# Performance work log

Hardware: AMD Instinct MI355X
Metric: run time of the kernel (lower is better)

Reference implementation:

```python
import jax, jax.numpy as jnp
from jax import lax
import numpy as np

B, T, C, H = 1024, 512, 32, 256


def _gru_cell(x, h, Wih, Whh, bih, bhh):
    # PyTorch GRU gate math. x: (B, C_in), h: (B, H)
    gi = x @ Wih.T + bih          # (B, 3H)
    gh = h @ Whh.T + bhh          # (B, 3H)
    i_r, i_z, i_n = jnp.split(gi, 3, axis=-1)
    h_r, h_z, h_n = jnp.split(gh, 3, axis=-1)
    r = jax.nn.sigmoid(i_r + h_r)
    z = jax.nn.sigmoid(i_z + h_z)
    n = jnp.tanh(i_n + r * h_n)
    return (1.0 - z) * n + z * h


def setup_inputs() -> dict:
    key = jax.random.key(0)
    ks = jax.random.split(key, 12)
    s = 0.08  # ~ uniform(-1/sqrt(H)) scale
    return {
        "x": jax.random.normal(ks[0], (B, T, C), dtype=jnp.float32),
        "enc_Wih": jax.random.normal(ks[1], (3 * H, C), dtype=jnp.float32) * s,
        "enc_Whh": jax.random.normal(ks[2], (3 * H, H), dtype=jnp.float32) * s,
        "enc_bih": jax.random.normal(ks[3], (3 * H,), dtype=jnp.float32) * s,
        "enc_bhh": jax.random.normal(ks[4], (3 * H,), dtype=jnp.float32) * s,
        "dec_Wih": jax.random.normal(ks[5], (3 * H, C), dtype=jnp.float32) * s,
        "dec_Whh": jax.random.normal(ks[6], (3 * H, H), dtype=jnp.float32) * s,
        "dec_bih": jax.random.normal(ks[7], (3 * H,), dtype=jnp.float32) * s,
        "dec_bhh": jax.random.normal(ks[8], (3 * H,), dtype=jnp.float32) * s,
        "proj_W": jax.random.normal(ks[9], (C, H), dtype=jnp.float32) * s,
        "proj_b": jax.random.normal(ks[10], (C,), dtype=jnp.float32) * s,
    }


def reference(x, enc_Wih, enc_Whh, enc_bih, enc_bhh,
              dec_Wih, dec_Whh, dec_bih, dec_bhh, proj_W, proj_b):
    batch = x.shape[0]
    h0 = jnp.zeros((batch, H), dtype=x.dtype)

    # ---- encoder: scan over time, keep only final hidden ----
    xs = jnp.swapaxes(x, 0, 1)  # (T, B, C)

    def enc_step(h, xt):
        return _gru_cell(xt, h, enc_Wih, enc_Whh, enc_bih, enc_bhh), None

    h_enc, _ = lax.scan(enc_step, h0, xs)

    start = jnp.zeros((batch, C), dtype=x.dtype)

    def dec_step(carry, _):
        h, prev = carry
        h_new = _gru_cell(prev, h, dec_Wih, dec_Whh, dec_bih, dec_bhh)
        pred = h_new @ proj_W.T + proj_b  # (B, C)
        return (h_new, pred), pred

    _, preds = lax.scan(dec_step, (h_enc, start), None, length=T)
    return jnp.swapaxes(preds, 0, 1)  # (B, T, C)
```

## Files before the change

kernel.cpp:

```cpp
#include <hip/hip_runtime.h>

typedef short bf16x8 __attribute__((ext_vector_type(8)));
typedef float f32x4 __attribute__((ext_vector_type(4)));

#define MFMA16(a, b, c) __builtin_amdgcn_mfma_f32_16x16x32_bf16(a, b, c, 0, 0, 0)

#define T_ 512
#define C_ 32
#define H_ 256

__device__ __forceinline__ unsigned short f2bf(float f) {
  union { float f; unsigned u; } v; v.f = f;
  return (unsigned short)((v.u + 0x7fffu + ((v.u >> 16) & 1u)) >> 16);
}
__device__ __forceinline__ float fsigmoid(float x) {
  float e = __builtin_amdgcn_exp2f(-1.442695041f * x);
  return __builtin_amdgcn_rcpf(1.0f + e);
}
__device__ __forceinline__ float ftanh(float x) {
  float e = __builtin_amdgcn_exp2f(2.885390082f * x);
  return 1.0f - 2.0f * __builtin_amdgcn_rcpf(e + 1.0f);
}

__global__ void pack_kernel(
    const float* __restrict__ encWih, const float* __restrict__ encWhh,
    const float* __restrict__ encbih, const float* __restrict__ encbhh,
    const float* __restrict__ decWih, const float* __restrict__ decWhh,
    const float* __restrict__ decbih, const float* __restrict__ decbhh,
    const float* __restrict__ projW, const float* __restrict__ projB,
    unsigned short* __restrict__ encW, unsigned short* __restrict__ decW,
    unsigned short* __restrict__ pW, float* __restrict__ encBias,
    float* __restrict__ decBias, float* __restrict__ pB) {
  int i = blockIdx.x * 256 + threadIdx.x;
  if (i < 768 * 288) {
    int n = i / 288, k = i % 288;
    float ve = (k < 32) ? encWih[n * 32 + k] : encWhh[n * 256 + k - 32];
    float vd = (k < 32) ? decWih[n * 32 + k] : decWhh[n * 256 + k - 32];
    encW[i] = f2bf(ve);
    decW[i] = f2bf(vd);
  }
  if (i < 32 * 256) pW[i] = f2bf(projW[i]);
  if (i < 256) {
    encBias[i]       = encbih[i] + encbhh[i];
    encBias[256 + i] = encbih[256 + i] + encbhh[256 + i];
    encBias[512 + i] = encbih[512 + i];
    encBias[768 + i] = encbhh[512 + i];
    decBias[i]       = decbih[i] + decbhh[i];
    decBias[256 + i] = decbih[256 + i] + decbhh[256 + i];
    decBias[512 + i] = decbih[512 + i];
    decBias[768 + i] = decbhh[512 + i];
  }
  if (i < 32) pB[i] = projB[i];
}

__global__ __launch_bounds__(1024) void gru_kernel(
    const float* __restrict__ x,
    const unsigned short* __restrict__ encW,
    const unsigned short* __restrict__ decW,
    const unsigned short* __restrict__ pW,
    const float* __restrict__ encBias,
    const float* __restrict__ decBias,
    const float* __restrict__ pB,
    float* __restrict__ out) {
  __shared__ __align__(16) unsigned short wnl[6][256][40];
  __shared__ __align__(16) unsigned short h_lds[2][16][264];
  __shared__ __align__(16) unsigned short xb[2][16][40];
  __shared__ __align__(16) unsigned short pwl[32][264];

  const int tid = (int)threadIdx.x;
  const int wave = tid >> 6, lane = tid & 63;
  const int l15 = lane & 15, l4 = lane >> 4;
  const int ko = l4 * 8;
  const int gbase = (int)blockIdx.x * 16;
  const int j = wave * 16 + l15;

  for (int i = tid; i < 2 * 16 * 264 / 2; i += 1024) ((unsigned*)h_lds)[i] = 0;
  for (int i = tid; i < 2 * 16 * 40 / 2; i += 1024) ((unsigned*)xb)[i] = 0;
  {
    int n = tid >> 5, slot = tid & 31;
    *(bf16x8*)&pwl[n][slot * 8] = *(const bf16x8*)(pW + n * 256 + slot * 8);
  }

  const float* xLane = x + (size_t)(gbase + (tid >> 5)) * (T_ * C_) + (tid & 31);
  float* outLane = out + (size_t)(gbase + l4 * 4) * (T_ * C_) + wave * 16 + l15;
  const float pbias = (wave < 2) ? pB[wave * 16 + l15] : 0.f;
  f32x4 hreg = {0.f, 0.f, 0.f, 0.f};

  bf16x8 wi0, wi1, wi2, wr[8], wz[8], wn2[2];

  auto loadW = [&](const unsigned short* Wp) {
    wi0 = *(const bf16x8*)(Wp + (size_t)j * 288 + ko);
    wi1 = *(const bf16x8*)(Wp + (size_t)(j + 256) * 288 + ko);
    wi2 = *(const bf16x8*)(Wp + (size_t)(j + 512) * 288 + ko);
#pragma unroll
    for (int kk = 0; kk < 8; ++kk) {
      wr[kk] = *(const bf16x8*)(Wp + (size_t)j * 288 + 32 + kk * 32 + ko);
      wz[kk] = *(const bf16x8*)(Wp + (size_t)(j + 256) * 288 + 32 + kk * 32 + ko);
    }
#pragma unroll
    for (int kk = 0; kk < 2; ++kk)
      wn2[kk] = *(const bf16x8*)(Wp + (size_t)(j + 512) * 288 + 32 + kk * 32 + ko);
    for (int i = tid; i < 6 * 256 * 4; i += 1024) {
      int kc = i >> 10, rem = i & 1023;
      int jj = rem >> 2, kc2 = rem & 3;
      *(bf16x8*)&wnl[kc][jj][kc2 * 8] =
          *(const bf16x8*)(Wp + (size_t)(jj + 512) * 288 + 32 + (kc + 2) * 32 + kc2 * 8);
    }
  };

  loadW(encW);
  float br = encBias[j], bz = encBias[256 + j];
  float bin = encBias[512 + j], bhn = encBias[768 + j];
  if (tid < 512) xb[0][tid >> 5][tid & 31] = f2bf(xLane[0]);
  __syncthreads();

  for (int t = 0; t < T_; ++t) {
    if (t < T_ - 1 && tid < 512)
      xb[(t + 1) & 1][tid >> 5][tid & 31] = f2bf(xLane[(size_t)(t + 1) * C_]);

    f32x4 accr = {br, br, br, br}, accz = {bz, bz, bz, bz};
    f32x4 accin = {bin, bin, bin, bin}, acchn = {bhn, bhn, bhn, bhn};
    {
      bf16x8 a0 = *(const bf16x8*)&xb[t & 1][l15][ko];
      accr  = MFMA16(a0, wi0, accr);
      accz  = MFMA16(a0, wi1, accz);
      accin = MFMA16(a0, wi2, accin);
    }
#pragma unroll
    for (int kk = 0; kk < 8; ++kk) {
      bf16x8 ah = *(const bf16x8*)&h_lds[t & 1][l15][kk * 32 + ko];
      accr = MFMA16(ah, wr[kk], accr);
      accz = MFMA16(ah, wz[kk], accz);
      bf16x8 wnk = (kk < 2) ? wn2[kk] : *(const bf16x8*)&wnl[kk - 2][j][ko];
      acchn = MFMA16(ah, wnk, acchn);
    }
#pragma unroll
    for (int r = 0; r < 4; ++r) {
      float rg = fsigmoid(accr[r]);
      float zg = fsigmoid(accz[r]);
      float ng = ftanh(accin[r] + rg * acchn[r]);
      float hv = zg * (hreg[r] - ng) + ng;
      hreg[r] = hv;
      h_lds[(t + 1) & 1][l4 * 4 + r][j] = f2bf(hv);
    }
    __syncthreads();
  }

  loadW(decW);
  br = decBias[j]; bz = decBias[256 + j];
  bin = decBias[512 + j]; bhn = decBias[768 + j];
  if (tid < 320) ((unsigned*)xb)[tid] = 0;
  __syncthreads();

  for (int t = 0; t < T_; ++t) {
    f32x4 accr = {br, br, br, br}, accz = {bz, bz, bz, bz};
    f32x4 accin = {bin, bin, bin, bin}, acchn = {bhn, bhn, bhn, bhn};
    {
      bf16x8 a0 = *(const bf16x8*)&xb[0][l15][ko];
      accr  = MFMA16(a0, wi0, accr);
      accz  = MFMA16(a0, wi1, accz);
      accin = MFMA16(a0, wi2, accin);
    }
#pragma unroll
    for (int kk = 0; kk < 8; ++kk) {
      bf16x8 ah = *(const bf16x8*)&h_lds[t & 1][l15][kk * 32 + ko];
      accr = MFMA16(ah, wr[kk], accr);
      accz = MFMA16(ah, wz[kk], accz);
      bf16x8 wnk = (kk < 2) ? wn2[kk] : *(const bf16x8*)&wnl[kk - 2][j][ko];
      acchn = MFMA16(ah, wnk, acchn);
    }
#pragma unroll
    for (int r = 0; r < 4; ++r) {
      float rg = fsigmoid(accr[r]);
      float zg = fsigmoid(accz[r]);
      float ng = ftanh(accin[r] + rg * acchn[r]);
      float hv = zg * (hreg[r] - ng) + ng;
      hreg[r] = hv;
      h_lds[(t + 1) & 1][l4 * 4 + r][j] = f2bf(hv);
    }
    __syncthreads();

    if (wave < 2) {
      f32x4 pa = {pbias, pbias, pbias, pbias};
#pragma unroll
      for (int kk = 0; kk < 8; ++kk) {
        bf16x8 ah = *(const bf16x8*)&h_lds[(t + 1) & 1][l15][kk * 32 + ko];
        bf16x8 bw = *(const bf16x8*)&pwl[wave * 16 + l15][kk * 32 + ko];
        pa = MFMA16(ah, bw, pa);
      }
#pragma unroll
      for (int r = 0; r < 4; ++r) {
        outLane[(size_t)r * (T_ * C_) + t * C_] = pa[r];
        xb[0][l4 * 4 + r][wave * 16 + l15] = f2bf(pa[r]);
      }
    }
    __syncthreads();
  }
}

extern "C" void kernel_launch(void* const* d_in, const int* in_sizes, int n_in,
                              void* d_out, int out_size, void* d_ws, size_t ws_size,
                              hipStream_t stream) {
  const float* x      = (const float*)d_in[0];
  const float* encWih = (const float*)d_in[1];
  const float* encWhh = (const float*)d_in[2];
  const float* encbih = (const float*)d_in[3];
  const float* encbhh = (const float*)d_in[4];
  const float* decWih = (const float*)d_in[5];
  const float* decWhh = (const float*)d_in[6];
  const float* decbih = (const float*)d_in[7];
  const float* decbhh = (const float*)d_in[8];
  const float* projW  = (const float*)d_in[9];
  const float* projB  = (const float*)d_in[10];

  char* ws = (char*)d_ws;
  unsigned short* encW = (unsigned short*)(ws);
  unsigned short* decW = (unsigned short*)(ws + 442368);
  unsigned short* pW   = (unsigned short*)(ws + 884736);
  float* encBias = (float*)(ws + 901120);
  float* decBias = (float*)(ws + 905216);
  float* pB      = (float*)(ws + 909312);

  pack_kernel<<<864, 256, 0, stream>>>(encWih, encWhh, encbih, encbhh,
                                       decWih, decWhh, decbih, decbhh,
                                       projW, projB,
                                       encW, decW, pW, encBias, decBias, pB);
  gru_kernel<<<64, 1024, 0, stream>>>(x, encW, decW, pW, encBias, decBias, pB,
                                      (float*)d_out);
}
```

Before: 2.484 ms.

## Halve block to 512 threads with two hidden-column tiles per wave

Each wave now computes two 16-column slices of the hidden state instead of one, so the block shrinks from 16 to 8 waves while covering the same 256 hidden units. This interleaves independent MFMA chains within a wave for more ILP and makes the per-step __syncthreads cheaper with fewer waves. One more n-gate weight chunk moves from LDS into registers, shrinking the LDS buffer. The cost is roughly double the register footprint per lane, which risks spilling, and only 8 waves per CU are left to hide latency.

```diff
diff --git a/kernel.cpp b/kernel.cpp
--- a/kernel.cpp
+++ b/kernel.cpp
@@ -53,7 +53,7 @@
   if (i < 32) pB[i] = projB[i];
 }
 
-__global__ __launch_bounds__(1024) void gru_kernel(
+__global__ __launch_bounds__(512, 2) void gru_kernel(
     const float* __restrict__ x,
     const unsigned short* __restrict__ encW,
     const unsigned short* __restrict__ decW,
@@ -62,7 +62,7 @@
     const float* __restrict__ decBias,
     const float* __restrict__ pB,
     float* __restrict__ out) {
-  __shared__ __align__(16) unsigned short wnl[6][256][40];
+  __shared__ __align__(16) unsigned short wnl[5][256][40];
   __shared__ __align__(16) unsigned short h_lds[2][16][264];
   __shared__ __align__(16) unsigned short xb[2][16][40];
   __shared__ __align__(16) unsigned short pwl[32][264];
@@ -72,111 +72,142 @@
   const int l15 = lane & 15, l4 = lane >> 4;
   const int ko = l4 * 8;
   const int gbase = (int)blockIdx.x * 16;
-  const int j = wave * 16 + l15;
-
-  for (int i = tid; i < 2 * 16 * 264 / 2; i += 1024) ((unsigned*)h_lds)[i] = 0;
-  for (int i = tid; i < 2 * 16 * 40 / 2; i += 1024) ((unsigned*)xb)[i] = 0;
-  {
-    int n = tid >> 5, slot = tid & 31;
+  const int j0 = wave * 32 + l15;
+  const int j1 = j0 + 16;
+
+  for (int i = tid; i < 2 * 16 * 264 / 2; i += 512) ((unsigned*)h_lds)[i] = 0;
+  for (int i = tid; i < 2 * 16 * 40 / 2; i += 512) ((unsigned*)xb)[i] = 0;
+  for (int i = tid; i < 1024; i += 512) {
+    int n = i >> 5, slot = i & 31;
     *(bf16x8*)&pwl[n][slot * 8] = *(const bf16x8*)(pW + n * 256 + slot * 8);
   }
 
   const float* xLane = x + (size_t)(gbase + (tid >> 5)) * (T_ * C_) + (tid & 31);
   float* outLane = out + (size_t)(gbase + l4 * 4) * (T_ * C_) + wave * 16 + l15;
   const float pbias = (wave < 2) ? pB[wave * 16 + l15] : 0.f;
-  f32x4 hreg = {0.f, 0.f, 0.f, 0.f};
-
-  bf16x8 wi0, wi1, wi2, wr[8], wz[8], wn2[2];
+  f32x4 hreg0 = {0.f, 0.f, 0.f, 0.f}, hreg1 = {0.f, 0.f, 0.f, 0.f};
+
+  bf16x8 wi0a, wi1a, wi2a, wra[8], wza[8], wna[3];
+  bf16x8 wi0b, wi1b, wi2b, wrb[8], wzb[8], wnb[3];
 
   auto loadW = [&](const unsigned short* Wp) {
-    wi0 = *(const bf16x8*)(Wp + (size_t)j * 288 + ko);
-    wi1 = *(const bf16x8*)(Wp + (size_t)(j + 256) * 288 + ko);
-    wi2 = *(const bf16x8*)(Wp + (size_t)(j + 512) * 288 + ko);
+    wi0a = *(const bf16x8*)(Wp + (size_t)j0 * 288 + ko);
+    wi1a = *(const bf16x8*)(Wp + (size_t)(j0 + 256) * 288 + ko);
+    wi2a = *(const bf16x8*)(Wp + (size_t)(j0 + 512) * 288 + ko);
+    wi0b = *(const bf16x8*)(Wp + (size_t)j1 * 288 + ko);
+    wi1b = *(const bf16x8*)(Wp + (size_t)(j1 + 256) * 288 + ko);
+    wi2b = *(const bf16x8*)(Wp + (size_t)(j1 + 512) * 288 + ko);
 #pragma unroll
     for (int kk = 0; kk < 8; ++kk) {
-      wr[kk] = *(const bf16x8*)(Wp + (size_t)j * 288 + 32 + kk * 32 + ko);
-      wz[kk] = *(const bf16x8*)(Wp + (size_t)(j + 256) * 288 + 32 + kk * 32 + ko);
-    }
-#pragma unroll
-    for (int kk = 0; kk < 2; ++kk)
-      wn2[kk] = *(const bf16x8*)(Wp + (size_t)(j + 512) * 288 + 32 + kk * 32 + ko);
-    for (int i = tid; i < 6 * 256 * 4; i += 1024) {
+      wra[kk] = *(const bf16x8*)(Wp + (size_t)j0 * 288 + 32 + kk * 32 + ko);
+      wza[kk] = *(const bf16x8*)(Wp + (size_t)(j0 + 256) * 288 + 32 + kk * 32 + ko);
+      wrb[kk] = *(const bf16x8*)(Wp + (size_t)j1 * 288 + 32 + kk * 32 + ko);
+      wzb[kk] = *(const bf16x8*)(Wp + (size_t)(j1 + 256) * 288 + 32 + kk * 32 + ko);
+    }
+#pragma unroll
+    for (int kk = 0; kk < 3; ++kk) {
+      wna[kk] = *(const bf16x8*)(Wp + (size_t)(j0 + 512) * 288 + 32 + kk * 32 + ko);
+      wnb[kk] = *(const bf16x8*)(Wp + (size_t)(j1 + 512) * 288 + 32 + kk * 32 + ko);
+    }
+    for (int i = tid; i < 5 * 256 * 4; i += 512) {
       int kc = i >> 10, rem = i & 1023;
       int jj = rem >> 2, kc2 = rem & 3;
       *(bf16x8*)&wnl[kc][jj][kc2 * 8] =
-          *(const bf16x8*)(Wp + (size_t)(jj + 512) * 288 + 32 + (kc + 2) * 32 + kc2 * 8);
+          *(const bf16x8*)(Wp + (size_t)(jj + 512) * 288 + 32 + (kc + 3) * 32 + kc2 * 8);
     }
   };
 
   loadW(encW);
-  float br = encBias[j], bz = encBias[256 + j];
-  float bin = encBias[512 + j], bhn = encBias[768 + j];
-  if (tid < 512) xb[0][tid >> 5][tid & 31] = f2bf(xLane[0]);
+  float br0 = encBias[j0], bz0 = encBias[256 + j0];
+  float bin0 = encBias[512 + j0], bhn0 = encBias[768 + j0];
+  float br1 = encBias[j1], bz1 = encBias[256 + j1];
+  float bin1 = encBias[512 + j1], bhn1 = encBias[768 + j1];
+  xb[0][tid >> 5][tid & 31] = f2bf(xLane[0]);
   __syncthreads();
 
   for (int t = 0; t < T_; ++t) {
-    if (t < T_ - 1 && tid < 512)
+    if (t < T_ - 1)
       xb[(t + 1) & 1][tid >> 5][tid & 31] = f2bf(xLane[(size_t)(t + 1) * C_]);
 
-    f32x4 accr = {br, br, br, br}, accz = {bz, bz, bz, bz};
-    f32x4 accin = {bin, bin, bin, bin}, acchn = {bhn, bhn, bhn, bhn};
+    f32x4 ar0 = {br0, br0, br0, br0}, az0 = {bz0, bz0, bz0, bz0};
+    f32x4 ain0 = {bin0, bin0, bin0, bin0}, ahn0 = {bhn0, bhn0, bhn0, bhn0};
+    f32x4 ar1 = {br1, br1, br1, br1}, az1 = {bz1, bz1, bz1, bz1};
+    f32x4 ain1 = {bin1, bin1, bin1, bin1}, ahn1 = {bhn1, bhn1, bhn1, bhn1};
     {
       bf16x8 a0 = *(const bf16x8*)&xb[t & 1][l15][ko];
-      accr  = MFMA16(a0, wi0, accr);
-      accz  = MFMA16(a0, wi1, accz);
-      accin = MFMA16(a0, wi2, accin);
+      ar0  = MFMA16(a0, wi0a, ar0);  ar1  = MFMA16(a0, wi0b, ar1);
+      az0  = MFMA16(a0, wi1a, az0);  az1  = MFMA16(a0, wi1b, az1);
+      ain0 = MFMA16(a0, wi2a, ain0); ain1 = MFMA16(a0, wi2b, ain1);
     }
 #pragma unroll
     for (int kk = 0; kk < 8; ++kk) {
       bf16x8 ah = *(const bf16x8*)&h_lds[t & 1][l15][kk * 32 + ko];
-      accr = MFMA16(ah, wr[kk], accr);
-      accz = MFMA16(ah, wz[kk], accz);
-      bf16x8 wnk = (kk < 2) ? wn2[kk] : *(const bf16x8*)&wnl[kk - 2][j][ko];
-      acchn = MFMA16(ah, wnk, acchn);
+      ar0 = MFMA16(ah, wra[kk], ar0);  ar1 = MFMA16(ah, wrb[kk], ar1);
+      az0 = MFMA16(ah, wza[kk], az0);  az1 = MFMA16(ah, wzb[kk], az1);
+      bf16x8 wn0 = (kk < 3) ? wna[kk] : *(const bf16x8*)&wnl[kk - 3][j0][ko];
+      bf16x8 wn1 = (kk < 3) ? wnb[kk] : *(const bf16x8*)&wnl[kk - 3][j1][ko];
+      ahn0 = MFMA16(ah, wn0, ahn0);    ahn1 = MFMA16(ah, wn1, ahn1);
     }
 #pragma unroll
     for (int r = 0; r < 4; ++r) {
-      float rg = fsigmoid(accr[r]);
-      float zg = fsigmoid(accz[r]);
-      float ng = ftanh(accin[r] + rg * acchn[r]);
-      float hv = zg * (hreg[r] - ng) + ng;
-      hreg[r] = hv;
-      h_lds[(t + 1) & 1][l4 * 4 + r][j] = f2bf(hv);
+      float rg = fsigmoid(ar0[r]);
+      float zg = fsigmoid(az0[r]);
+      float ng = ftanh(ain0[r] + rg * ahn0[r]);
+      float hv = zg * (hreg0[r] - ng) + ng;
+      hreg0[r] = hv;
+      h_lds[(t + 1) & 1][l4 * 4 + r][j0] = f2bf(hv);
+      rg = fsigmoid(ar1[r]);
+      zg = fsigmoid(az1[r]);
+      ng = ftanh(ain1[r] + rg * ahn1[r]);
+      hv = zg * (hreg1[r] - ng) + ng;
+      hreg1[r] = hv;
+      h_lds[(t + 1) & 1][l4 * 4 + r][j1] = f2bf(hv);
     }
     __syncthreads();
   }
 
   loadW(decW);
-  br = decBias[j]; bz = decBias[256 + j];
-  bin = decBias[512 + j]; bhn = decBias[768 + j];
+  br0 = decBias[j0]; bz0 = decBias[256 + j0];
+  bin0 = decBias[512 + j0]; bhn0 = decBias[768 + j0];
+  br1 = decBias[j1]; bz1 = decBias[256 + j1];
+  bin1 = decBias[512 + j1]; bhn1 = decBias[768 + j1];
   if (tid < 320) ((unsigned*)xb)[tid] = 0;
   __syncthreads();
 
   for (int t = 0; t < T_; ++t) {
-    f32x4 accr = {br, br, br, br}, accz = {bz, bz, bz, bz};
-    f32x4 accin = {bin, bin, bin, bin}, acchn = {bhn, bhn, bhn, bhn};
+    f32x4 ar0 = {br0, br0, br0, br0}, az0 = {bz0, bz0, bz0, bz0};
+    f32x4 ain0 = {bin0, bin0, bin0, bin0}, ahn0 = {bhn0, bhn0, bhn0, bhn0};
+    f32x4 ar1 = {br1, br1, br1, br1}, az1 = {bz1, bz1, bz1, bz1};
+    f32x4 ain1 = {bin1, bin1, bin1, bin1}, ahn1 = {bhn1, bhn1, bhn1, bhn1};
     {
       bf16x8 a0 = *(const bf16x8*)&xb[0][l15][ko];
-      accr  = MFMA16(a0, wi0, accr);
-      accz  = MFMA16(a0, wi1, accz);
-      accin = MFMA16(a0, wi2, accin);
+      ar0  = MFMA16(a0, wi0a, ar0);  ar1  = MFMA16(a0, wi0b, ar1);
+      az0  = MFMA16(a0, wi1a, az0);  az1  = MFMA16(a0, wi1b, az1);
+      ain0 = MFMA16(a0, wi2a, ain0); ain1 = MFMA16(a0, wi2b, ain1);
     }
 #pragma unroll
     for (int kk = 0; kk < 8; ++kk) {
       bf16x8 ah = *(const bf16x8*)&h_lds[t & 1][l15][kk * 32 + ko];
-      accr = MFMA16(ah, wr[kk], accr);
-      accz = MFMA16(ah, wz[kk], accz);
-      bf16x8 wnk = (kk < 2) ? wn2[kk] : *(const bf16x8*)&wnl[kk - 2][j][ko];
-      acchn = MFMA16(ah, wnk, acchn);
+      ar0 = MFMA16(ah, wra[kk], ar0);  ar1 = MFMA16(ah, wrb[kk], ar1);
+      az0 = MFMA16(ah, wza[kk], az0);  az1 = MFMA16(ah, wzb[kk], az1);
+      bf16x8 wn0 = (kk < 3) ? wna[kk] : *(const bf16x8*)&wnl[kk - 3][j0][ko];
+      bf16x8 wn1 = (kk < 3) ? wnb[kk] : *(const bf16x8*)&wnl[kk - 3][j1][ko];
+      ahn0 = MFMA16(ah, wn0, ahn0);    ahn1 = MFMA16(ah, wn1, ahn1);
     }
 #pragma unroll
     for (int r = 0; r < 4; ++r) {
-      float rg = fsigmoid(accr[r]);
-      float zg = fsigmoid(accz[r]);
-      float ng = ftanh(accin[r] + rg * acchn[r]);
-      float hv = zg * (hreg[r] - ng) + ng;
-      hreg[r] = hv;
-      h_lds[(t + 1) & 1][l4 * 4 + r][j] = f2bf(hv);
+      float rg = fsigmoid(ar0[r]);
+      float zg = fsigmoid(az0[r]);
+      float ng = ftanh(ain0[r] + rg * ahn0[r]);
+      float hv = zg * (hreg0[r] - ng) + ng;
+      hreg0[r] = hv;
+      h_lds[(t + 1) & 1][l4 * 4 + r][j0] = f2bf(hv);
+      rg = fsigmoid(ar1[r]);
+      zg = fsigmoid(az1[r]);
+      ng = ftanh(ain1[r] + rg * ahn1[r]);
+      hv = zg * (hreg1[r] - ng) + ng;
+      hreg1[r] = hv;
+      h_lds[(t + 1) & 1][l4 * 4 + r][j1] = f2bf(hv);
     }
     __syncthreads();
 
@@ -225,6 +256,6 @@
                                        decWih, decWhh, decbih, decbhh,
                                        projW, projB,
                                        encW, decW, pW, encBias, decBias, pB);
-  gru_kernel<<<64, 1024, 0, stream>>>(x, encW, decW, pW, encBias, decBias, pB,
-                                      (float*)d_out);
-}
+  gru_kernel<<<64, 512, 0, stream>>>(x, encW, decW, pW, encBias, decBias, pB,
+                                     (float*)d_out);
+}
```

After: 2.615 ms. 5.3% more time.

## Overlap decoder projection with hidden matmul and fold activation scales into weights

Applied to the files above, without the earlier changes.

The decoder step is reordered so the recurrent h·Whh MFMAs for step t run in the same phase as the projection of the previous hidden state. The input-gate MFMAs are deferred until the projected prediction is available. This shortens the serial dependency chain per step, though it still needs two barriers per step. Separately, the exp2 scaling constants for the sigmoid and tanh gates are pre-multiplied into the packed bf16 weights and biases, which removes a multiply per activation but changes bf16 rounding slightly.

```diff
diff --git a/kernel.cpp b/kernel.cpp
--- a/kernel.cpp
+++ b/kernel.cpp
@@ -12,14 +12,6 @@
 __device__ __forceinline__ unsigned short f2bf(float f) {
   union { float f; unsigned u; } v; v.f = f;
   return (unsigned short)((v.u + 0x7fffu + ((v.u >> 16) & 1u)) >> 16);
-}
-__device__ __forceinline__ float fsigmoid(float x) {
-  float e = __builtin_amdgcn_exp2f(-1.442695041f * x);
-  return __builtin_amdgcn_rcpf(1.0f + e);
-}
-__device__ __forceinline__ float ftanh(float x) {
-  float e = __builtin_amdgcn_exp2f(2.885390082f * x);
-  return 1.0f - 2.0f * __builtin_amdgcn_rcpf(e + 1.0f);
 }
 
 __global__ void pack_kernel(
@@ -31,24 +23,27 @@
     unsigned short* __restrict__ encW, unsigned short* __restrict__ decW,
     unsigned short* __restrict__ pW, float* __restrict__ encBias,
     float* __restrict__ decBias, float* __restrict__ pB) {
+  const float SRZ = -1.442695041f;
+  const float SN  = 2.885390082f;
   int i = blockIdx.x * 256 + threadIdx.x;
   if (i < 768 * 288) {
     int n = i / 288, k = i % 288;
+    float sc = (n < 512) ? SRZ : SN;
     float ve = (k < 32) ? encWih[n * 32 + k] : encWhh[n * 256 + k - 32];
     float vd = (k < 32) ? decWih[n * 32 + k] : decWhh[n * 256 + k - 32];
-    encW[i] = f2bf(ve);
-    decW[i] = f2bf(vd);
+    encW[i] = f2bf(ve * sc);
+    decW[i] = f2bf(vd * sc);
   }
   if (i < 32 * 256) pW[i] = f2bf(projW[i]);
   if (i < 256) {
-    encBias[i]       = encbih[i] + encbhh[i];
-    encBias[256 + i] = encbih[256 + i] + encbhh[256 + i];
-    encBias[512 + i] = encbih[512 + i];
-    encBias[768 + i] = encbhh[512 + i];
-    decBias[i]       = decbih[i] + decbhh[i];
-    decBias[256 + i] = decbih[256 + i] + decbhh[256 + i];
-    decBias[512 + i] = decbih[512 + i];
-    decBias[768 + i] = decbhh[512 + i];
+    encBias[i]       = (encbih[i] + encbhh[i]) * SRZ;
+    encBias[256 + i] = (encbih[256 + i] + encbhh[256 + i]) * SRZ;
+    encBias[512 + i] = encbih[512 + i] * SN;
+    encBias[768 + i] = encbhh[512 + i] * SN;
+    decBias[i]       = (decbih[i] + decbhh[i]) * SRZ;
+    decBias[256 + i] = (decbih[256 + i] + decbhh[256 + i]) * SRZ;
+    decBias[512 + i] = decbih[512 + i] * SN;
+    decBias[768 + i] = decbhh[512 + i] * SN;
   }
   if (i < 32) pB[i] = projB[i];
 }
@@ -108,6 +103,20 @@
     }
   };
 
+  auto gates_store = [&](const f32x4& accr, const f32x4& accz,
+                         const f32x4& accin, const f32x4& acchn, int buf) {
+#pragma unroll
+    for (int r = 0; r < 4; ++r) {
+      float rg = __builtin_amdgcn_rcpf(1.0f + __builtin_amdgcn_exp2f(accr[r]));
+      float zg = __builtin_amdgcn_rcpf(1.0f + __builtin_amdgcn_exp2f(accz[r]));
+      float ng = 1.0f - 2.0f * __builtin_amdgcn_rcpf(
+                              1.0f + __builtin_amdgcn_exp2f(accin[r] + rg * acchn[r]));
+      float h = zg * (hreg[r] - ng) + ng;
+      hreg[r] = h;
+      h_lds[buf][l4 * 4 + r][j] = f2bf(h);
+    }
+  };
+
   loadW(encW);
   float br = encBias[j], bz = encBias[256 + j];
   float bin = encBias[512 + j], bhn = encBias[768 + j];
@@ -134,15 +143,7 @@
       bf16x8 wnk = (kk < 2) ? wn2[kk] : *(const bf16x8*)&wnl[kk - 2][j][ko];
       acchn = MFMA16(ah, wnk, acchn);
     }
-#pragma unroll
-    for (int r = 0; r < 4; ++r) {
-      float rg = fsigmoid(accr[r]);
-      float zg = fsigmoid(accz[r]);
-      float ng = ftanh(accin[r] + rg * acchn[r]);
-      float hv = zg * (hreg[r] - ng) + ng;
-      hreg[r] = hv;
-      h_lds[(t + 1) & 1][l4 * 4 + r][j] = f2bf(hv);
-    }
+    gates_store(accr, accz, accin, acchn, (t + 1) & 1);
     __syncthreads();
   }
 
@@ -153,48 +154,55 @@
   __syncthreads();
 
   for (int t = 0; t < T_; ++t) {
+    const int p = t & 1;
     f32x4 accr = {br, br, br, br}, accz = {bz, bz, bz, bz};
     f32x4 accin = {bin, bin, bin, bin}, acchn = {bhn, bhn, bhn, bhn};
-    {
-      bf16x8 a0 = *(const bf16x8*)&xb[0][l15][ko];
-      accr  = MFMA16(a0, wi0, accr);
-      accz  = MFMA16(a0, wi1, accz);
-      accin = MFMA16(a0, wi2, accin);
-    }
-#pragma unroll
-    for (int kk = 0; kk < 8; ++kk) {
-      bf16x8 ah = *(const bf16x8*)&h_lds[t & 1][l15][kk * 32 + ko];
+    f32x4 pa = {pbias, pbias, pbias, pbias};
+#pragma unroll
+    for (int kk = 0; kk < 8; ++kk) {
+      bf16x8 ah = *(const bf16x8*)&h_lds[p][l15][kk * 32 + ko];
       accr = MFMA16(ah, wr[kk], accr);
       accz = MFMA16(ah, wz[kk], accz);
       bf16x8 wnk = (kk < 2) ? wn2[kk] : *(const bf16x8*)&wnl[kk - 2][j][ko];
       acchn = MFMA16(ah, wnk, acchn);
     }
-#pragma unroll
-    for (int r = 0; r < 4; ++r) {
-      float rg = fsigmoid(accr[r]);
-      float zg = fsigmoid(accz[r]);
-      float ng = ftanh(accin[r] + rg * acchn[r]);
-      float hv = zg * (hreg[r] - ng) + ng;
-      hreg[r] = hv;
-      h_lds[(t + 1) & 1][l4 * 4 + r][j] = f2bf(hv);
-    }
-    __syncthreads();
-
-    if (wave < 2) {
-      f32x4 pa = {pbias, pbias, pbias, pbias};
+    if (t > 0 && wave < 2) {
 #pragma unroll
       for (int kk = 0; kk < 8; ++kk) {
-        bf16x8 ah = *(const bf16x8*)&h_lds[(t + 1) & 1][l15][kk * 32 + ko];
+        bf16x8 ah = *(const bf16x8*)&h_lds[p][l15][kk * 32 + ko];
         bf16x8 bw = *(const bf16x8*)&pwl[wave * 16 + l15][kk * 32 + ko];
         pa = MFMA16(ah, bw, pa);
       }
+      const int n = wave * 16 + l15;
 #pragma unroll
       for (int r = 0; r < 4; ++r) {
-        outLane[(size_t)r * (T_ * C_) + t * C_] = pa[r];
-        xb[0][l4 * 4 + r][wave * 16 + l15] = f2bf(pa[r]);
+        outLane[(size_t)r * (T_ * C_) + (t - 1) * C_] = pa[r];
+        xb[p][l4 * 4 + r][n] = f2bf(pa[r]);
       }
     }
     __syncthreads();
+
+    {
+      bf16x8 a0 = *(const bf16x8*)&xb[p][l15][ko];
+      accr  = MFMA16(a0, wi0, accr);
+      accz  = MFMA16(a0, wi1, accz);
+      accin = MFMA16(a0, wi2, accin);
+    }
+    gates_store(accr, accz, accin, acchn, p ^ 1);
+    __syncthreads();
+  }
+
+  if (wave < 2) {
+    f32x4 pa = {pbias, pbias, pbias, pbias};
+#pragma unroll
+    for (int kk = 0; kk < 8; ++kk) {
+      bf16x8 ah = *(const bf16x8*)&h_lds[0][l15][kk * 32 + ko];
+      bf16x8 bw = *(const bf16x8*)&pwl[wave * 16 + l15][kk * 32 + ko];
+      pa = MFMA16(ah, bw, pa);
+    }
+#pragma unroll
+    for (int r = 0; r < 4; ++r)
+      outLane[(size_t)r * (T_ * C_) + 511 * C_] = pa[r];
   }
 }
 
```

Measured after the change: 3.940 ms. +58.6%, slower.
